# Kernel optimization log

Measured on AMD Instinct MI355X. Metric: run time of the kernel, lower is better.

## Reference

```python
import jax, jax.numpy as jnp
import numpy as np
from jax import lax

DN = ('NCHW', 'OIHW', 'NCHW')
NUM_IN_CAPS = 1152  # 32 * 6 * 6
NUM_OUT_CAPS = 10
IN_CAP_DIM = 8
OUT_CAP_DIM = 16
ROUTING_ITERS = 3


def squash(x):
    # unit_v * |x|^2 / (1 + |x|^2), norm over last dim
    n = jnp.linalg.norm(x, axis=-1, keepdims=True)
    return (x / n) * (n * n / (1.0 + n * n))


def setup_inputs() -> dict:
    key = jax.random.key(0)
    ks = jax.random.split(key, 12)
    B = 256
    return {
        'x': jax.random.normal(ks[0], (B, 1, 28, 28), jnp.float32),
        'conv1_w': jax.random.normal(ks[1], (256, 1, 9, 9), jnp.float32) * 0.05,
        'conv1_b': jnp.zeros((256,), jnp.float32),
        'pconv_w': jax.random.normal(ks[2], (256, 256, 9, 9), jnp.float32) * 0.02,
        'pconv_b': jnp.zeros((256,), jnp.float32),
        'W_caps': jax.random.normal(ks[3], (NUM_IN_CAPS, NUM_OUT_CAPS, OUT_CAP_DIM, IN_CAP_DIM), jnp.float32),
        'dec_w1': jax.random.normal(ks[4], (160, 512), jnp.float32) * 0.05,
        'dec_b1': jnp.zeros((512,), jnp.float32),
        'dec_w2': jax.random.normal(ks[5], (512, 1024), jnp.float32) * 0.04,
        'dec_b2': jnp.zeros((1024,), jnp.float32),
        'dec_w3': jax.random.normal(ks[6], (1024, 784), jnp.float32) * 0.03,
        'dec_b3': jnp.zeros((784,), jnp.float32),
    }


def reference(x, conv1_w, conv1_b, pconv_w, pconv_b, W_caps,
              dec_w1, dec_b1, dec_w2, dec_b2, dec_w3, dec_b3):
    # conv1: 1 -> 256, k9, s1, no activation (faithful to source)
    h = lax.conv_general_dilated(x, conv1_w, (1, 1), 'VALID', dimension_numbers=DN)
    h = h + conv1_b[None, :, None, None]  # (B,256,20,20)
    # primary caps conv: 256 -> 32*8, k9, s2
    h = lax.conv_general_dilated(h, pconv_w, (2, 2), 'VALID', dimension_numbers=DN)
    h = h + pconv_b[None, :, None, None]  # (B,256,6,6)
    B = h.shape[0]
    u_in = squash(h.reshape(B, -1, IN_CAP_DIM))  # (B,1152,8)
    # prediction vectors u_hat: (B,1152,10,16)
    u = jnp.einsum('ijab,nib->nija', W_caps, u_in)
    # routing-by-agreement; b is shared across batch and accumulates batch-summed agreement (faithful)
    b = jnp.zeros((NUM_IN_CAPS, NUM_OUT_CAPS), u.dtype)
    v = None
    for r in range(ROUTING_ITERS + 1):
        c = jax.nn.softmax(b, axis=-1)             # (1152,10)
        s = jnp.einsum('ij,nija->nja', c, u)        # (B,10,16)
        v = squash(s)
        if r < ROUTING_ITERS:
            b = b + jnp.einsum('nija,nja->ij', u, v)
    # decoder path: mask by predicted class
    logits = jnp.linalg.norm(v, axis=-1)            # (B,10)
    label = jnp.argmax(logits, axis=1)
    one_hot = jax.nn.one_hot(label, NUM_OUT_CAPS, dtype=v.dtype)
    recon = (one_hot[..., None] * v).reshape(B, NUM_OUT_CAPS * OUT_CAP_DIM)
    recon = jax.nn.relu(recon @ dec_w1 + dec_b1)
    recon = jax.nn.relu(recon @ dec_w2 + dec_b2)
    recon = jax.nn.sigmoid(recon @ dec_w3 + dec_b3)  # (B,784)
    return (v, recon)
```

## Files before the change

### kernel.cpp

```cpp
#include <hip/hip_runtime.h>
#include <hip/hip_fp16.h>
#include <math.h>


typedef __attribute__((ext_vector_type(8))) _Float16 half8;
typedef __attribute__((ext_vector_type(8))) short short8;
typedef __attribute__((ext_vector_type(4))) float floatx4;

__device__ __forceinline__ unsigned short f16bits(float v) {
    _Float16 h = (_Float16)v;
    unsigned short b;
    __builtin_memcpy(&b, &h, 2);
    return b;
}
__device__ __forceinline__ float f16back(unsigned short b) {
    _Float16 h;
    __builtin_memcpy(&h, &b, 2);
    return (float)h;
}
__device__ __forceinline__ void load_lds16(const void* g, void* l) {
    __builtin_amdgcn_global_load_lds(
        (const __attribute__((address_space(1))) unsigned int*)g,
        (__attribute__((address_space(3))) unsigned int*)l, 16, 0, 0);
}

__global__ __launch_bounds__(256, 2) void conv1_kernel(
    const float* __restrict__ x, const float* __restrict__ w,
    const float* __restrict__ bias, unsigned short* __restrict__ xpack)
{
    __shared__ float xs[784];
    __shared__ float wl[64 * 81];
    int t = threadIdx.x;
    int n = blockIdx.x;
    int cot = blockIdx.y;

    for (int j = t; j < 784; j += 256) xs[j] = x[n * 784 + j];
    {
        int co_s = t >> 2, k0 = (t & 3) * 21;
        const float* wsrc = w + (size_t)(cot * 64 + co_s) * 81;
        #pragma unroll
        for (int k = 0; k < 21; ++k)
            if (k0 + k < 81) wl[co_s * 81 + k0 + k] = wsrc[k0 + k];
    }
    __syncthreads();

    int co_l = t & 63, slot = t >> 6;
    int co = cot * 64 + co_l;
    float bv = bias[co];
    for (int r5 = 0; r5 < 5; ++r5) {
        int py = slot * 5 + r5;
        float acc[20];
        #pragma unroll
        for (int i = 0; i < 20; i++) acc[i] = bv;
        #pragma unroll
        for (int ky = 0; ky < 9; ++ky) {
            float xr[28];
            const float4* rowp = (const float4*)&xs[(py + ky) * 28];
            #pragma unroll
            for (int q = 0; q < 7; q++) {
                float4 v4 = rowp[q];
                xr[4*q] = v4.x; xr[4*q+1] = v4.y; xr[4*q+2] = v4.z; xr[4*q+3] = v4.w;
            }
            #pragma unroll
            for (int kx = 0; kx < 9; ++kx) {
                float wv = wl[co_l * 81 + ky * 9 + kx];
                #pragma unroll
                for (int px = 0; px < 20; ++px) acc[px] += wv * xr[px + kx];
            }
        }
        #pragma unroll
        for (int px = 0; px < 20; ++px) {
            float v = acc[px];
            unsigned short h = f16bits(v);
            unsigned short l = f16bits(v - f16back(h));
            size_t pix = (size_t)n * 400 + py * 20 + px;
            xpack[pix * 512 + co] = h;
            xpack[pix * 512 + 256 + co] = l;
        }
    }
}

__global__ __launch_bounds__(256) void wpack_kernel(
    const float* __restrict__ w, unsigned short* __restrict__ wp)
{
    int tid = blockIdx.x * 256 + threadIdx.x;
    if (tid >= 648 * 16 * 64) return;
    int lane = tid & 63, g = (tid >> 6) & 15, gs = tid >> 10;
    int cb = gs & 7, kk = gs >> 3;
    int ky = kk / 9, kx = kk - ky * 9;
    int n16 = lane & 15, q = lane >> 4;
    int co = g * 16 + n16;
    unsigned short hv[8];
    #pragma unroll
    for (int j = 0; j < 8; ++j) {
        int ci = cb * 32 + q * 8 + j;
        hv[j] = f16bits(w[((size_t)co * 256 + ci) * 81 + ky * 9 + kx]);
    }
    unsigned short* dst = wp + ((size_t)gs * 16 + g) * 512 + lane * 8;
    *(short8*)dst = *(short8*)hv;
}

__global__ __launch_bounds__(256, 2) void pconv_mfma_kernel(
    const unsigned short* __restrict__ xp, const unsigned short* __restrict__ wp,
    __half* __restrict__ P3)
{
    __shared__ unsigned char lds[32768];
    int t = threadIdx.x;
    int lane = t & 63;
    int w = __builtin_amdgcn_readfirstlane(t >> 6);
    int mtile = blockIdx.x, kc = blockIdx.y;
    int m16 = lane & 15, q = lane >> 4;

    unsigned int asrc[2];
    #pragma unroll
    for (int j = 0; j < 2; ++j) {
        int r = w * 16 + j * 8 + (lane >> 3);
        int m = mtile * 64 + r;
        int n = m / 36, pos = m - n * 36;
        int oy = pos / 6, ox = pos - oy * 6;
        int pixbase = n * 400 + oy * 40 + ox * 2;
        int pp = (lane & 7) ^ (lane >> 3);
        int partoff = (pp < 4) ? pp * 16 : 512 + (pp - 4) * 16;
        asrc[j] = (unsigned int)(pixbase * 1024 + partoff);
    }
    const char* xb = (const char*)xp;
    const char* wb = (const char*)wp;

    floatx4 acc[4][4];
    #pragma unroll
    for (int a = 0; a < 4; ++a)
        #pragma unroll
        for (int b = 0; b < 4; ++b) acc[a][b] = (floatx4){0.f, 0.f, 0.f, 0.f};

    int slot_hi = (q ^ (m16 & 7)) * 16;
    int slot_lo = slot_hi ^ 64;

    auto stageP = [&](int p, int buf) {
        #pragma unroll
        for (int e = 0; e < 2; ++e) {
            int s = 2 * p + e; if (s > 215) s = 215;
            int gs = kc * 216 + s;
            int kk = gs >> 3, cb = gs & 7;
            int ky = kk / 9, kx = kk - ky * 9;
            unsigned int delta = (unsigned int)((ky * 20 + kx) * 1024 + cb * 64);
            #pragma unroll
            for (int j = 0; j < 2; ++j)
                load_lds16(xb + asrc[j] + delta,
                           (void*)(lds + buf * 16384 + e * 8192 + w * 2048 + j * 1024));
        }
    };
    auto loadB = [&](int s, half8* B) {
        if (s > 215) s = 215;
        int gs = kc * 216 + s;
        #pragma unroll
        for (int c = 0; c < 4; ++c)
            B[c] = *(const half8*)(wb + ((size_t)gs * 16 + (w * 4 + c)) * 1024 + lane * 16);
    };
    auto compute = [&](int buf, int e, half8* B) {
        #pragma unroll
        for (int ms = 0; ms < 4; ++ms) {
            const char* base = (const char*)lds + buf * 16384 + e * 8192 + (ms * 16 + m16) * 128;
            half8 Ah = *(const half8*)(base + slot_hi);
            half8 Al = *(const half8*)(base + slot_lo);
            #pragma unroll
            for (int c = 0; c < 4; ++c) {
                acc[ms][c] = __builtin_amdgcn_mfma_f32_16x16x32_f16(Ah, B[c], acc[ms][c], 0, 0, 0);
                acc[ms][c] = __builtin_amdgcn_mfma_f32_16x16x32_f16(Al, B[c], acc[ms][c], 0, 0, 0);
            }
        }
    };

    half8 Bcur[4], Bnext[4];
    stageP(0, 0);
    loadB(0, Bcur);
    __syncthreads();
    for (int p = 0; p < 108; ++p) {
        int buf = p & 1;
        stageP(p + 1, buf ^ 1);
        loadB(2 * p + 1, Bnext);
        compute(buf, 0, Bcur);
        loadB(2 * p + 2, Bcur);
        compute(buf, 1, Bnext);
        __syncthreads();
    }

    __half* outp = P3 + ((size_t)kc * 9216 + (size_t)mtile * 64) * 256;
    #pragma unroll
    for (int ms = 0; ms < 4; ++ms)
        #pragma unroll
        for (int r = 0; r < 4; ++r) {
            int ml = ms * 16 + q * 4 + r;
            #pragma unroll
            for (int c = 0; c < 4; ++c) {
                int co = w * 64 + c * 16 + m16;
                outp[ml * 256 + co] = __float2half(acc[ms][c][r]);
            }
        }
}

__global__ __launch_bounds__(256) void squash_u_kernel(
    const __half* __restrict__ P3, const float* __restrict__ pb, float* __restrict__ u)
{
    int cap = blockIdx.x * 256 + threadIdx.x;
    int n = cap / 1152;
    int capl = cap - n * 1152;
    float z[8]; float n2 = 0.f;
    #pragma unroll
    for (int b = 0; b < 8; ++b) {
        int q2 = capl * 8 + b;
        int co = q2 / 36;
        int pos = q2 - co * 36;
        int m = n * 36 + pos;
        float s = 0.f;
        #pragma unroll
        for (int kc = 0; kc < 3; ++kc)
            s += __half2float(P3[((size_t)kc * 9216 + m) * 256 + co]);
        s += pb[co];
        z[b] = s; n2 += s * s;
    }
    float sc = sqrtf(n2) / (1.0f + n2);
    float4* op = (float4*)(u + (size_t)cap * 8);
    op[0] = make_float4(z[0]*sc, z[1]*sc, z[2]*sc, z[3]*sc);
    op[1] = make_float4(z[4]*sc, z[5]*sc, z[6]*sc, z[7]*sc);
}

__global__ __launch_bounds__(256, 2) void s_kernel(
    const float* __restrict__ b, const float* __restrict__ u,
    const float* __restrict__ W, float* __restrict__ sbuf)
{
    __shared__ float cs[24][10];
    int t = threadIdx.x;
    int a = t & 15, nl = t >> 4;
    int nt = blockIdx.x;
    int bz = blockIdx.y;
    int i0 = bz * 24;
    int n0 = nt * 32 + nl * 2;

    if (t < 24) {
        int i = i0 + t;
        float e[10], m = -1e30f;
        #pragma unroll
        for (int j = 0; j < 10; j++) { e[j] = b[i * 10 + j]; m = fmaxf(m, e[j]); }
        float sum = 0.f;
        #pragma unroll
        for (int j = 0; j < 10; j++) { e[j] = expf(e[j] - m); sum += e[j]; }
        float inv = 1.f / sum;
        #pragma unroll
        for (int j = 0; j < 10; j++) cs[t][j] = e[j] * inv;
    }
    __syncthreads();

    float acc[2][10];
    #pragma unroll
    for (int r = 0; r < 2; ++r)
        #pragma unroll
        for (int j = 0; j < 10; ++j) acc[r][j] = 0.f;

    for (int i = i0; i < i0 + 24; ++i) {
        float4 u0[2], u1[2];
        #pragma unroll
        for (int r = 0; r < 2; ++r) {
            const float4* up = (const float4*)&u[(size_t)(n0 + r) * 9216 + (size_t)i * 8];
            u0[r] = up[0]; u1[r] = up[1];
        }
        #pragma unroll
        for (int j = 0; j < 10; ++j) {
            const float4* wpt = (const float4*)&W[(((size_t)i * 10 + j) * 16 + a) * 8];
            float4 w0 = wpt[0], w1 = wpt[1];
            float cij = cs[i - i0][j];
            #pragma unroll
            for (int r = 0; r < 2; ++r) {
                float d = w0.x*u0[r].x + w0.y*u0[r].y + w0.z*u0[r].z + w0.w*u0[r].w
                        + w1.x*u1[r].x + w1.y*u1[r].y + w1.z*u1[r].z + w1.w*u1[r].w;
                acc[r][j] += cij * d;
            }
        }
    }
    #pragma unroll
    for (int r = 0; r < 2; ++r)
        #pragma unroll
        for (int j = 0; j < 10; ++j)
            sbuf[(size_t)bz * 40960 + (((size_t)(n0 + r) * 10 + j) * 16) + a] = acc[r][j];
}

__global__ __launch_bounds__(256) void squash_v_kernel(const float* __restrict__ sbuf,
                                float* __restrict__ v, float* __restrict__ vout)
{
    int t = threadIdx.x;
    int a = t & 15;
    int idx = blockIdx.x * 16 + (t >> 4);
    float s = 0.f;
    #pragma unroll
    for (int z = 0; z < 48; ++z) s += sbuf[(size_t)z * 40960 + idx * 16 + a];
    float n2 = s * s;
    n2 += __shfl_xor(n2, 1);
    n2 += __shfl_xor(n2, 2);
    n2 += __shfl_xor(n2, 4);
    n2 += __shfl_xor(n2, 8);
    float sc = sqrtf(n2) / (1.0f + n2);
    float y = s * sc;
    v[idx * 16 + a] = y;
    if (vout) vout[idx * 16 + a] = y;
}

__global__ __launch_bounds__(192) void bupd_kernel(
    const float* __restrict__ u, const float* __restrict__ v,
    const float* __restrict__ W, float* __restrict__ b)
{
    int i0 = blockIdx.x * 4;
    int n0 = blockIdx.y * 128;
    int t = threadIdx.x;
    if (t >= 160) return;
    int j = t >> 4, a = t & 15;
    float g4[4][8];
    #pragma unroll
    for (int g = 0; g < 4; ++g)
        #pragma unroll
        for (int k = 0; k < 8; ++k) g4[g][k] = 0.f;

    for (int n = n0; n < n0 + 128; ++n) {
        float vv = v[n * 160 + t];
        const float4* ub = (const float4*)&u[(size_t)n * 9216 + (size_t)i0 * 8];
        #pragma unroll
        for (int g = 0; g < 4; ++g) {
            float4 q0 = ub[g * 2], q1 = ub[g * 2 + 1];
            g4[g][0] += q0.x * vv; g4[g][1] += q0.y * vv; g4[g][2] += q0.z * vv; g4[g][3] += q0.w * vv;
            g4[g][4] += q1.x * vv; g4[g][5] += q1.y * vv; g4[g][6] += q1.z * vv; g4[g][7] += q1.w * vv;
        }
    }
    #pragma unroll
    for (int g = 0; g < 4; ++g) {
        int i = i0 + g;
        const float4* wpt = (const float4*)&W[(((size_t)i * 10 + j) * 16 + a) * 8];
        float4 w0 = wpt[0], w1 = wpt[1];
        float p = w0.x*g4[g][0] + w0.y*g4[g][1] + w0.z*g4[g][2] + w0.w*g4[g][3]
                + w1.x*g4[g][4] + w1.y*g4[g][5] + w1.z*g4[g][6] + w1.w*g4[g][7];
        p += __shfl_xor(p, 1);
        p += __shfl_xor(p, 2);
        p += __shfl_xor(p, 4);
        p += __shfl_xor(p, 8);
        if (a == 0) atomicAdd(&b[i * 10 + j], p);
    }
}

__global__ void mask_kernel(const float* __restrict__ v, float* __restrict__ out)
{
    int n = threadIdx.x;
    const float* vp = &v[n * 160];
    int best = 0; float bestv = -1.f;
    for (int j = 0; j < 10; j++) {
        float n2 = 0.f;
        #pragma unroll
        for (int a = 0; a < 16; a++) { float y = vp[j * 16 + a]; n2 += y * y; }
        float ln = sqrtf(n2);
        if (ln > bestv) { bestv = ln; best = j; }
    }
    for (int j = 0; j < 10; j++)
        for (int a = 0; a < 16; a++)
            out[n * 160 + j * 16 + a] = (j == best) ? vp[j * 16 + a] : 0.f;
}

template<int K, int KCH, int O>
__global__ __launch_bounds__(256, 2) void mlp_part_kernel(
    const float* __restrict__ X, const float* __restrict__ Wm,
    float* __restrict__ partial)
{
    __shared__ float XS[KCH * 16];
    int t = threadIdx.x;
    int og = t & 63, ns = t >> 6;
    int n0 = blockIdx.x * 16;
    int o = blockIdx.y * 256 + og * 4;
    int o_c = min(o, O - 4);
    int ks = blockIdx.z;
    int kc0 = ks * KCH;

    for (int idx = t; idx < KCH * 16; idx += 256) {
        int k_l = idx >> 4, n_l = idx & 15;
        XS[k_l * 16 + n_l] = X[(size_t)(n0 + n_l) * K + kc0 + k_l];
    }
    __syncthreads();

    float acc[4][4];
    #pragma unroll
    for (int r = 0; r < 4; ++r)
        #pragma unroll
        for (int q = 0; q < 4; ++q) acc[r][q] = 0.f;

    #pragma unroll 8
    for (int k = 0; k < KCH; ++k) {
        float4 wv = *(const float4*)&Wm[(size_t)(kc0 + k) * O + o_c];
        float4 xs4 = *(const float4*)&XS[k * 16 + ns * 4];
        acc[0][0] += xs4.x * wv.x; acc[0][1] += xs4.x * wv.y; acc[0][2] += xs4.x * wv.z; acc[0][3] += xs4.x * wv.w;
        acc[1][0] += xs4.y * wv.x; acc[1][1] += xs4.y * wv.y; acc[1][2] += xs4.y * wv.z; acc[1][3] += xs4.y * wv.w;
        acc[2][0] += xs4.z * wv.x; acc[2][1] += xs4.z * wv.y; acc[2][2] += xs4.z * wv.z; acc[2][3] += xs4.z * wv.w;
        acc[3][0] += xs4.w * wv.x; acc[3][1] += xs4.w * wv.y; acc[3][2] += xs4.w * wv.z; acc[3][3] += xs4.w * wv.w;
    }

    if (o < O) {
        float* pp = partial + ((size_t)ks * 256 + n0 + ns * 4) * O + o;
        #pragma unroll
        for (int r = 0; r < 4; ++r)
            *(float4*)(pp + (size_t)r * O) = make_float4(acc[r][0], acc[r][1], acc[r][2], acc[r][3]);
    }
}

template<int KS, int O, int ACT>
__global__ __launch_bounds__(256) void mlp_reduce_kernel(
    const float* __restrict__ partial, const float* __restrict__ bias,
    float* __restrict__ out)
{
    int n = blockIdx.y;
    int o = (blockIdx.x * 256 + threadIdx.x) * 4;
    if (o >= O) return;
    float4 s = make_float4(0.f, 0.f, 0.f, 0.f);
    #pragma unroll
    for (int ks = 0; ks < KS; ++ks) {
        float4 p = *(const float4*)&partial[((size_t)ks * 256 + n) * O + o];
        s.x += p.x; s.y += p.y; s.z += p.z; s.w += p.w;
    }
    float4 bv = *(const float4*)&bias[o];
    float r[4] = {s.x + bv.x, s.y + bv.y, s.z + bv.z, s.w + bv.w};
    #pragma unroll
    for (int q = 0; q < 4; ++q)
        r[q] = (ACT == 0) ? fmaxf(r[q], 0.f) : (1.f / (1.f + expf(-r[q])));
    *(float4*)&out[(size_t)n * O + o] = make_float4(r[0], r[1], r[2], r[3]);
}

extern "C" void kernel_launch(void* const* d_in, const int* in_sizes, int n_in,
                              void* d_out, int out_size, void* d_ws, size_t ws_size,
                              hipStream_t stream)
{
    const float* x       = (const float*)d_in[0];
    const float* conv1_w = (const float*)d_in[1];
    const float* conv1_b = (const float*)d_in[2];
    const float* pconv_w = (const float*)d_in[3];
    const float* pconv_b = (const float*)d_in[4];
    const float* W_caps  = (const float*)d_in[5];
    const float* dec_w1  = (const float*)d_in[6];
    const float* dec_b1  = (const float*)d_in[7];
    const float* dec_w2  = (const float*)d_in[8];
    const float* dec_b2  = (const float*)d_in[9];
    const float* dec_w3  = (const float*)d_in[10];
    const float* dec_b3  = (const float*)d_in[11];
    float* out = (float*)d_out;

    float* ws = (float*)d_ws;
    size_t off = 0;
    auto alloc = [&](size_t nf) { float* p = ws + off; off += (nf + 63) & ~(size_t)63; return p; };
    unsigned short* xpack = (unsigned short*)alloc(26214400);
    unsigned short* wpack = (unsigned short*)alloc(2654208);
    __half* P3  = (__half*)alloc(3538944);
    float* u_in = alloc(2359296);
    float* bbuf = alloc(11520);
    float* sbuf = alloc(48 * 40960);
    float* vbuf = alloc(40960);
    float* rin  = alloc(40960);
    float* mpart = alloc(8 * 256 * 1024);
    float* h1   = alloc(131072);
    float* h2   = alloc(262144);

    hipMemsetAsync(bbuf, 0, 11520 * sizeof(float), stream);

    wpack_kernel<<<(648 * 16 * 64 + 255) / 256, 256, 0, stream>>>(pconv_w, wpack);
    conv1_kernel<<<dim3(256, 4), 256, 0, stream>>>(x, conv1_w, conv1_b, xpack);
    pconv_mfma_kernel<<<dim3(144, 3), 256, 0, stream>>>(xpack, wpack, P3);
    squash_u_kernel<<<1152, 256, 0, stream>>>(P3, pconv_b, u_in);

    for (int r = 0; r < 4; ++r) {
        s_kernel<<<dim3(8, 48), 256, 0, stream>>>(bbuf, u_in, W_caps, sbuf);
        squash_v_kernel<<<160, 256, 0, stream>>>(sbuf, vbuf, (r == 3) ? out : nullptr);
        if (r < 3) bupd_kernel<<<dim3(288, 2), 192, 0, stream>>>(u_in, vbuf, W_caps, bbuf);
    }

    mask_kernel<<<1, 256, 0, stream>>>(vbuf, rin);

    mlp_part_kernel<160, 80, 512><<<dim3(16, 2, 2), 256, 0, stream>>>(rin, dec_w1, mpart);
    mlp_reduce_kernel<2, 512, 0><<<dim3(1, 256), 256, 0, stream>>>(mpart, dec_b1, h1);
    mlp_part_kernel<512, 128, 1024><<<dim3(16, 4, 4), 256, 0, stream>>>(h1, dec_w2, mpart);
    mlp_reduce_kernel<4, 1024, 0><<<dim3(1, 256), 256, 0, stream>>>(mpart, dec_b2, h2);
    mlp_part_kernel<1024, 128, 784><<<dim3(16, 4, 8), 256, 0, stream>>>(h2, dec_w3, mpart);
    mlp_reduce_kernel<8, 784, 1><<<dim3(1, 256), 256, 0, stream>>>(mpart, dec_b3, out + 40960);
}
```

Before: 763.6 us.

## Double split-K in primary caps conv and parallelize the mask kernel

Measured after the change: 744.7 us. -2.5%, faster.

```diff
diff --git a/kernel.cpp b/kernel.cpp
--- a/kernel.cpp
+++ b/kernel.cpp
@@ -100,9 +100,9 @@
     *(short8*)dst = *(short8*)hv;
 }
 
-__global__ __launch_bounds__(256, 2) void pconv_mfma_kernel(
+__global__ __launch_bounds__(256, 3) void pconv_mfma_kernel(
     const unsigned short* __restrict__ xp, const unsigned short* __restrict__ wp,
-    __half* __restrict__ P3)
+    __half* __restrict__ P6)
 {
     __shared__ unsigned char lds[32768];
     int t = threadIdx.x;
@@ -138,8 +138,8 @@
     auto stageP = [&](int p, int buf) {
         #pragma unroll
         for (int e = 0; e < 2; ++e) {
-            int s = 2 * p + e; if (s > 215) s = 215;
-            int gs = kc * 216 + s;
+            int s = 2 * p + e; if (s > 107) s = 107;
+            int gs = kc * 108 + s;
             int kk = gs >> 3, cb = gs & 7;
             int ky = kk / 9, kx = kk - ky * 9;
             unsigned int delta = (unsigned int)((ky * 20 + kx) * 1024 + cb * 64);
@@ -150,8 +150,8 @@
         }
     };
     auto loadB = [&](int s, half8* B) {
-        if (s > 215) s = 215;
-        int gs = kc * 216 + s;
+        if (s > 107) s = 107;
+        int gs = kc * 108 + s;
         #pragma unroll
         for (int c = 0; c < 4; ++c)
             B[c] = *(const half8*)(wb + ((size_t)gs * 16 + (w * 4 + c)) * 1024 + lane * 16);
@@ -170,21 +170,22 @@
         }
     };
 
-    half8 Bcur[4], Bnext[4];
+    half8 B0[4], B1[4], B2[4], B3[4];
     stageP(0, 0);
-    loadB(0, Bcur);
+    loadB(0, B0); loadB(1, B1);
     __syncthreads();
-    for (int p = 0; p < 108; ++p) {
-        int buf = p & 1;
-        stageP(p + 1, buf ^ 1);
-        loadB(2 * p + 1, Bnext);
-        compute(buf, 0, Bcur);
-        loadB(2 * p + 2, Bcur);
-        compute(buf, 1, Bnext);
+    for (int p = 0; p < 54; p += 2) {
+        stageP(p + 1, 1);
+        loadB(2 * p + 2, B2); loadB(2 * p + 3, B3);
+        compute(0, 0, B0); compute(0, 1, B1);
         __syncthreads();
-    }
-
-    __half* outp = P3 + ((size_t)kc * 9216 + (size_t)mtile * 64) * 256;
+        stageP(p + 2, 0);
+        loadB(2 * p + 4, B0); loadB(2 * p + 5, B1);
+        compute(1, 0, B2); compute(1, 1, B3);
+        __syncthreads();
+    }
+
+    __half* outp = P6 + ((size_t)kc * 9216 + (size_t)mtile * 64) * 256;
     #pragma unroll
     for (int ms = 0; ms < 4; ++ms)
         #pragma unroll
@@ -199,7 +200,7 @@
 }
 
 __global__ __launch_bounds__(256) void squash_u_kernel(
-    const __half* __restrict__ P3, const float* __restrict__ pb, float* __restrict__ u)
+    const __half* __restrict__ P6, const float* __restrict__ pb, float* __restrict__ u)
 {
     int cap = blockIdx.x * 256 + threadIdx.x;
     int n = cap / 1152;
@@ -213,8 +214,8 @@
         int m = n * 36 + pos;
         float s = 0.f;
         #pragma unroll
-        for (int kc = 0; kc < 3; ++kc)
-            s += __half2float(P3[((size_t)kc * 9216 + m) * 256 + co]);
+        for (int kc = 0; kc < 6; ++kc)
+            s += __half2float(P6[((size_t)kc * 9216 + m) * 256 + co]);
         s += pb[co];
         z[b] = s; n2 += s * s;
     }
@@ -343,21 +344,26 @@
     }
 }
 
-__global__ void mask_kernel(const float* __restrict__ v, float* __restrict__ out)
-{
-    int n = threadIdx.x;
+__global__ __launch_bounds__(256) void mask_kernel(const float* __restrict__ v, float* __restrict__ out)
+{
+    int t = threadIdx.x;
+    int a = t & 15, nl = t >> 4;
+    int n = blockIdx.x * 16 + nl;
     const float* vp = &v[n * 160];
-    int best = 0; float bestv = -1.f;
-    for (int j = 0; j < 10; j++) {
-        float n2 = 0.f;
-        #pragma unroll
-        for (int a = 0; a < 16; a++) { float y = vp[j * 16 + a]; n2 += y * y; }
-        float ln = sqrtf(n2);
-        if (ln > bestv) { bestv = ln; best = j; }
-    }
-    for (int j = 0; j < 10; j++)
-        for (int a = 0; a < 16; a++)
-            out[n * 160 + j * 16 + a] = (j == best) ? vp[j * 16 + a] : 0.f;
+    int best = 0; float bestn2 = -1.f;
+    #pragma unroll
+    for (int j = 0; j < 10; ++j) {
+        float y = vp[j * 16 + a];
+        float n2 = y * y;
+        n2 += __shfl_xor(n2, 1);
+        n2 += __shfl_xor(n2, 2);
+        n2 += __shfl_xor(n2, 4);
+        n2 += __shfl_xor(n2, 8);
+        if (n2 > bestn2) { bestn2 = n2; best = j; }
+    }
+    #pragma unroll
+    for (int j = 0; j < 10; ++j)
+        out[n * 160 + j * 16 + a] = (j == best) ? vp[j * 16 + a] : 0.f;
 }
 
 template<int K, int KCH, int O>
@@ -449,7 +455,7 @@
     auto alloc = [&](size_t nf) { float* p = ws + off; off += (nf + 63) & ~(size_t)63; return p; };
     unsigned short* xpack = (unsigned short*)alloc(26214400);
     unsigned short* wpack = (unsigned short*)alloc(2654208);
-    __half* P3  = (__half*)alloc(3538944);
+    __half* P6  = (__half*)alloc(7077888);
     float* u_in = alloc(2359296);
     float* bbuf = alloc(11520);
     float* sbuf = alloc(48 * 40960);
@@ -463,8 +469,8 @@
 
     wpack_kernel<<<(648 * 16 * 64 + 255) / 256, 256, 0, stream>>>(pconv_w, wpack);
     conv1_kernel<<<dim3(256, 4), 256, 0, stream>>>(x, conv1_w, conv1_b, xpack);
-    pconv_mfma_kernel<<<dim3(144, 3), 256, 0, stream>>>(xpack, wpack, P3);
-    squash_u_kernel<<<1152, 256, 0, stream>>>(P3, pconv_b, u_in);
+    pconv_mfma_kernel<<<dim3(144, 6), 256, 0, stream>>>(xpack, wpack, P6);
+    squash_u_kernel<<<1152, 256, 0, stream>>>(P6, pconv_b, u_in);
 
     for (int r = 0; r < 4; ++r) {
         s_kernel<<<dim3(8, 48), 256, 0, stream>>>(bbuf, u_in, W_caps, sbuf);
@@ -472,7 +478,7 @@
         if (r < 3) bupd_kernel<<<dim3(288, 2), 192, 0, stream>>>(u_in, vbuf, W_caps, bbuf);
     }
 
-    mask_kernel<<<1, 256, 0, stream>>>(vbuf, rin);
+    mask_kernel<<<16, 256, 0, stream>>>(vbuf, rin);
 
     mlp_part_kernel<160, 80, 512><<<dim3(16, 2, 2), 256, 0, stream>>>(rin, dec_w1, mpart);
     mlp_reduce_kernel<2, 512, 0><<<dim3(1, 256), 256, 0, stream>>>(mpart, dec_b1, h1);
```
